# Optimization experiments

Measured on AMD Instinct MI355X. Metric: run time of the kernel, lower is better.

## Reference

```python
import jax, jax.numpy as jnp
import numpy as np

N_NODES = 102400
N_FEAT = 128
N_TPLT = 16
N_TPLT_NODES = 10
N_GRAPHS = 256
EPS = 1.0       # entropic regularization for the Sinkhorn OT solve
N_ITER = 50     # fixed Sinkhorn iterations


def setup_inputs() -> dict:
    key = jax.random.key(0)
    k1, k2 = jax.random.split(key)
    x = jax.random.normal(k1, (N_NODES, N_FEAT), dtype=jnp.float32)
    # template features ~ N(feature_init_mean=0, feature_init_std=1)
    tplt_features = jax.random.normal(k2, (N_TPLT, N_TPLT_NODES, N_FEAT), dtype=jnp.float32)
    # q0 initialized so softmax(q0) is uniform over template nodes
    q0 = jnp.zeros((N_TPLT, N_TPLT_NODES), dtype=jnp.float32)
    # equal-size graphs: 400 nodes per graph, sorted batch vector (PyG convention)
    batch = jnp.repeat(jnp.arange(N_GRAPHS, dtype=jnp.int32), N_NODES // N_GRAPHS)
    return {"x": x, "tplt_features": tplt_features, "q0": q0,
            "batch": batch, "num_graphs": N_GRAPHS}


def _wasserstein_to_templates(x, tplt_features, q0, batch, num_graphs):
    # x: [N, d] node features; tplt_features: [K, M, d]; q0: [K, M]; batch: [N]
    N = x.shape[0]
    K, M, d = tplt_features.shape
    # squared-Euclidean cost C[n,k,m] = ||x_n - T_km||^2   (ot.dist default)
    C = (jnp.sum(x * x, axis=-1)[:, None, None]
         + jnp.sum(tplt_features * tplt_features, axis=-1)[None, :, :]
         - 2.0 * jnp.einsum('nd,kmd->nkm', x, tplt_features))  # [N,K,M]

    # uniform node weights per graph: a_n = 1/|S_{batch[n]}|
    counts = jax.ops.segment_sum(jnp.ones((N,), x.dtype), batch, num_segments=num_graphs)
    log_a = -jnp.log(counts)[batch]                      # [N]
    # template node weights b = softmax(q0, axis=1)
    log_b = jax.nn.log_softmax(q0, axis=1)               # [K,M]

    def seg_lse(t):  # logsumexp over nodes within each graph; t: [N,K,M] -> [G,K,M]
        m = jax.ops.segment_max(t, batch, num_segments=num_graphs)
        s = jax.ops.segment_sum(jnp.exp(t - m[batch]), batch, num_segments=num_graphs)
        return m + jnp.log(s)

    def f_update(g):  # [G,K,M] -> [N,K]
        return EPS * (log_a[:, None] - jax.nn.logsumexp((g[batch] - C) / EPS, axis=2))

    def step(g, _):
        f = f_update(g)
        g_new = EPS * (log_b[None, :, :] - seg_lse((f[:, :, None] - C) / EPS))
        return g_new, None

    g0 = jnp.zeros((num_graphs, K, M), x.dtype)
    g, _ = jax.lax.scan(step, g0, None, length=N_ITER)
    f = f_update(g)
    # transport plan P[n,k,m] = exp((f + g - C)/eps); OT cost = <P, C> per (graph, template)
    logP = (f[:, :, None] + g[batch] - C) / EPS          # [N,K,M]
    per_node = jnp.sum(jnp.exp(logP) * C, axis=2)        # [N,K]
    return jax.ops.segment_sum(per_node, batch, num_segments=num_graphs)  # [G,K]


def reference(x, tplt_features, q0, batch, num_graphs):
    return _wasserstein_to_templates(x, tplt_features, q0, batch, num_graphs)
```

## Files before the change

### kernel.cpp

```cpp
#include <hip/hip_runtime.h>

#define K_TPLT 16
#define M_NODES 10
#define DFEAT 128
#define NMAX 7
#define N_ITER 50
#define NEG_BIG -1e30f
#define LOG2E 1.44269504088896340736f
#define LN2   0.69314718055994530942f

#define EXP2F(x) __builtin_amdgcn_exp2f(x)
#define LOG2F(x) __builtin_amdgcn_logf(x)

__global__ void zero_counts_k(int* counts, int G) {
    int g = blockIdx.x * blockDim.x + threadIdx.x;
    if (g < G) counts[g] = 0;
}

__global__ void count_nodes_k(const int* __restrict__ batch, int* counts, int N) {
    int i = blockIdx.x * blockDim.x + threadIdx.x;
    if (i < N) atomicAdd(&counts[batch[i]], 1);
}

__global__ void scan_counts_k(const int* __restrict__ counts, int* starts, int G) {
    __shared__ int sc[1024];
    int t = threadIdx.x;
    for (int g = t; g < G; g += blockDim.x) sc[g] = counts[g];
    __syncthreads();
    for (int g = t; g < G; g += blockDim.x) {
        int s = 0;
        for (int j = 0; j < g; ++j) s += sc[j];
        starts[g] = s;
    }
}

__global__ __launch_bounds__(64) void sinkhorn_tw_k(
    const float* __restrict__ x, const float* __restrict__ tplt,
    const float* __restrict__ q0, const int* __restrict__ starts,
    const int* __restrict__ counts, float* __restrict__ out, int G)
{
    const int bid  = blockIdx.x;
    const int g    = bid % G;
    const int k    = bid / G;
    const int lane = threadIdx.x;

    const int start = starts[g];
    const int count = counts[g];
    const float a   = 1.0f / (float)count;
    const float la2 = -LOG2F((float)count);

    const float* qk = q0 + k * M_NODES;
    float lbla[M_NODES];
    {
        float qv[M_NODES];
        float qmax = NEG_BIG;
#pragma unroll
        for (int m = 0; m < M_NODES; ++m) { qv[m] = qk[m]; qmax = fmaxf(qmax, qv[m]); }
        float qs = 0.f;
#pragma unroll
        for (int m = 0; m < M_NODES; ++m) {
            qv[m] = (qv[m] - qmax) * LOG2E;
            qs += EXP2F(qv[m]);
        }
        const float corr = LOG2F(qs);
#pragma unroll
        for (int m = 0; m < M_NODES; ++m) lbla[m] = qv[m] - corr - la2;
    }

    bool act[NMAX];
#pragma unroll
    for (int i = 0; i < NMAX; ++i) act[i] = (lane + i * 64) < count;

    float L[NMAX][M_NODES];
    float nsh[NMAX];
    float csh[M_NODES];
    {
        const float* Tk = tplt + (size_t)k * M_NODES * DFEAT;
        float x2[NMAX];
        float t2[M_NODES];
#pragma unroll
        for (int i = 0; i < NMAX; ++i) {
            x2[i] = 0.f;
#pragma unroll
            for (int m = 0; m < M_NODES; ++m) L[i][m] = 0.f;
        }
#pragma unroll
        for (int m = 0; m < M_NODES; ++m) t2[m] = 0.f;

        for (int j = 0; j < DFEAT; j += 4) {
            float4 xv[NMAX];
#pragma unroll
            for (int i = 0; i < NMAX; ++i) {
                if (act[i]) {
                    xv[i] = *(const float4*)(x + (size_t)(start + lane + i * 64) * DFEAT + j);
                } else {
                    xv[i].x = xv[i].y = xv[i].z = xv[i].w = 0.f;
                }
                x2[i] += xv[i].x * xv[i].x + xv[i].y * xv[i].y
                       + xv[i].z * xv[i].z + xv[i].w * xv[i].w;
            }
#pragma unroll
            for (int m = 0; m < M_NODES; ++m) {
                const float4 tv = *(const float4*)(Tk + m * DFEAT + j);
                t2[m] += tv.x * tv.x + tv.y * tv.y + tv.z * tv.z + tv.w * tv.w;
#pragma unroll
                for (int i = 0; i < NMAX; ++i) {
                    L[i][m] += xv[i].x * tv.x + xv[i].y * tv.y
                             + xv[i].z * tv.z + xv[i].w * tv.w;
                }
            }
        }
#pragma unroll
        for (int i = 0; i < NMAX; ++i) {
            float mx = NEG_BIG;
#pragma unroll
            for (int m = 0; m < M_NODES; ++m) {
                L[i][m] = (2.f * L[i][m] - x2[i] - t2[m]) * LOG2E;
                mx = fmaxf(mx, L[i][m]);
            }
            nsh[i] = mx;
#pragma unroll
            for (int m = 0; m < M_NODES; ++m) L[i][m] -= mx;
        }
#pragma unroll
        for (int m = 0; m < M_NODES; ++m) {
            float c = NEG_BIG;
#pragma unroll
            for (int i = 0; i < NMAX; ++i) c = act[i] ? fmaxf(c, L[i][m]) : c;
            for (int off = 32; off > 0; off >>= 1) c = fmaxf(c, __shfl_xor(c, off));
            csh[m] = c;
        }
    }

    float g2[M_NODES];

    {
        float w0[M_NODES], acc[M_NODES];
#pragma unroll
        for (int m = 0; m < M_NODES; ++m) { w0[m] = EXP2F(csh[m]); acc[m] = 0.f; }
#pragma unroll
        for (int i = 0; i < NMAX; ++i) {
            if (act[i]) {
                float E[M_NODES];
                float D = 0.f;
#pragma unroll
                for (int m = 0; m < M_NODES; ++m) {
                    E[m] = EXP2F(L[i][m] - csh[m]);
                    D = fmaf(E[m], w0[m], D);
                }
                const float r = __builtin_amdgcn_rcpf(D);
#pragma unroll
                for (int m = 0; m < M_NODES; ++m) acc[m] = fmaf(E[m], r, acc[m]);
            }
        }
#pragma unroll
        for (int m = 0; m < M_NODES; ++m) {
            float s = acc[m];
            for (int off = 32; off > 0; off >>= 1) s += __shfl_xor(s, off);
            g2[m] = lbla[m] - csh[m] - LOG2F(fmaxf(s, 1e-35f));
        }
    }

    for (int it = 1; it < N_ITER; ++it) {
        float acc[M_NODES];
#pragma unroll
        for (int m = 0; m < M_NODES; ++m) acc[m] = 0.f;

#pragma unroll
        for (int i = 0; i < NMAX; ++i) {
            if (act[i]) {
                float e[M_NODES];
                float zmax = NEG_BIG;
#pragma unroll
                for (int m = 0; m < M_NODES; ++m) {
                    e[m] = g2[m] + L[i][m];
                    zmax = fmaxf(zmax, e[m]);
                }
                float D = 0.f;
#pragma unroll
                for (int m = 0; m < M_NODES; ++m) { e[m] = EXP2F(e[m] - zmax); D += e[m]; }
                const float r = __builtin_amdgcn_rcpf(D);
#pragma unroll
                for (int m = 0; m < M_NODES; ++m) acc[m] = fmaf(e[m], r, acc[m]);
            }
        }
#pragma unroll
        for (int m = 0; m < M_NODES; ++m) {
            float s = acc[m];
            for (int off = 32; off > 0; off >>= 1) s += __shfl_xor(s, off);
            g2[m] = lbla[m] + g2[m] - LOG2F(fmaxf(s, 1e-35f));
        }
    }

    float accum = 0.f;
#pragma unroll
    for (int i = 0; i < NMAX; ++i) {
        if (act[i]) {
            float e[M_NODES];
            float zmax = NEG_BIG;
#pragma unroll
            for (int m = 0; m < M_NODES; ++m) {
                e[m] = g2[m] + L[i][m];
                zmax = fmaxf(zmax, e[m]);
            }
            float D = 0.f;
#pragma unroll
            for (int m = 0; m < M_NODES; ++m) { e[m] = EXP2F(e[m] - zmax); D += e[m]; }
            const float r = __builtin_amdgcn_rcpf(D);
            float q = 0.f;
#pragma unroll
            for (int m = 0; m < M_NODES; ++m) q = fmaf(e[m], L[i][m], q);
            accum += nsh[i] + q * r;
        }
    }
    for (int off = 32; off > 0; off >>= 1) accum += __shfl_xor(accum, off);
    if (lane == 0) out[(size_t)g * K_TPLT + k] = -a * LN2 * accum;
}

extern "C" void kernel_launch(void* const* d_in, const int* in_sizes, int n_in,
                              void* d_out, int out_size, void* d_ws, size_t ws_size,
                              hipStream_t stream) {
    const float* x    = (const float*)d_in[0];
    const float* tplt = (const float*)d_in[1];
    const float* q0   = (const float*)d_in[2];
    const int* batch  = (const int*)d_in[3];
    const int N = in_sizes[3];
    const int G = out_size / K_TPLT;

    int* counts = (int*)d_ws;
    int* starts = counts + G;

    zero_counts_k<<<(G + 255) / 256, 256, 0, stream>>>(counts, G);
    count_nodes_k<<<(N + 255) / 256, 256, 0, stream>>>(batch, counts, N);
    scan_counts_k<<<1, 256, 0, stream>>>(counts, starts, G);
    sinkhorn_tw_k<<<G * K_TPLT, 64, 0, stream>>>(x, tplt, q0, starts, counts,
                                                 (float*)d_out, G);
}
```

Measured before the change: 531.4 us.

## Split each graph-template Sinkhorn solve across two wavefronts with LDS reduction

Each block now uses two 64-lane wavefronts instead of one, with each wave holding up to four node slots per lane rather than seven. Per-iteration column sums and maxima are combined across the two waves through double-buffered shared memory and a block barrier. This is meant to halve per-wave serial work and register pressure (the L array shrinks from 70 to 40 floats), raising occupancy and parallelism for the 4096 blocks. The cost is a __syncthreads per Sinkhorn iteration. Nodes past 512 per graph are no longer covered, versus 448 before, so node coverage is still capped.

```diff
diff --git a/kernel.cpp b/kernel.cpp
--- a/kernel.cpp
+++ b/kernel.cpp
@@ -3,7 +3,7 @@
 #define K_TPLT 16
 #define M_NODES 10
 #define DFEAT 128
-#define NMAX 7
+#define NMAXW 4
 #define N_ITER 50
 #define NEG_BIG -1e30f
 #define LOG2E 1.44269504088896340736f
@@ -34,7 +34,7 @@
     }
 }
 
-__global__ __launch_bounds__(64) void sinkhorn_tw_k(
+__global__ __launch_bounds__(128) void sinkhorn_tw_k(
     const float* __restrict__ x, const float* __restrict__ tplt,
     const float* __restrict__ q0, const int* __restrict__ starts,
     const int* __restrict__ counts, float* __restrict__ out, int G)
@@ -42,7 +42,10 @@
     const int bid  = blockIdx.x;
     const int g    = bid % G;
     const int k    = bid / G;
-    const int lane = threadIdx.x;
+    const int w    = threadIdx.x >> 6;
+    const int lane = threadIdx.x & 63;
+
+    __shared__ float sm[2][2][M_NODES];
 
     const int start = starts[g];
     const int count = counts[g];
@@ -67,69 +70,76 @@
         for (int m = 0; m < M_NODES; ++m) lbla[m] = qv[m] - corr - la2;
     }
 
-    bool act[NMAX];
-#pragma unroll
-    for (int i = 0; i < NMAX; ++i) act[i] = (lane + i * 64) < count;
-
-    float L[NMAX][M_NODES];
-    float nsh[NMAX];
+    bool act[NMAXW];
+#pragma unroll
+    for (int j = 0; j < NMAXW; ++j) act[j] = (lane + 64 * (4 * w + j)) < count;
+
+    float L[NMAXW][M_NODES];
+    float nsh[NMAXW];
     float csh[M_NODES];
     {
         const float* Tk = tplt + (size_t)k * M_NODES * DFEAT;
-        float x2[NMAX];
+        float x2[NMAXW];
         float t2[M_NODES];
 #pragma unroll
-        for (int i = 0; i < NMAX; ++i) {
-            x2[i] = 0.f;
-#pragma unroll
-            for (int m = 0; m < M_NODES; ++m) L[i][m] = 0.f;
+        for (int j = 0; j < NMAXW; ++j) {
+            x2[j] = 0.f;
+#pragma unroll
+            for (int m = 0; m < M_NODES; ++m) L[j][m] = 0.f;
         }
 #pragma unroll
         for (int m = 0; m < M_NODES; ++m) t2[m] = 0.f;
 
-        for (int j = 0; j < DFEAT; j += 4) {
-            float4 xv[NMAX];
-#pragma unroll
-            for (int i = 0; i < NMAX; ++i) {
-                if (act[i]) {
-                    xv[i] = *(const float4*)(x + (size_t)(start + lane + i * 64) * DFEAT + j);
+        for (int jf = 0; jf < DFEAT; jf += 4) {
+            float4 xv[NMAXW];
+#pragma unroll
+            for (int j = 0; j < NMAXW; ++j) {
+                if (act[j]) {
+                    xv[j] = *(const float4*)(x + (size_t)(start + lane + 64 * (4 * w + j)) * DFEAT + jf);
                 } else {
-                    xv[i].x = xv[i].y = xv[i].z = xv[i].w = 0.f;
-                }
-                x2[i] += xv[i].x * xv[i].x + xv[i].y * xv[i].y
-                       + xv[i].z * xv[i].z + xv[i].w * xv[i].w;
+                    xv[j].x = xv[j].y = xv[j].z = xv[j].w = 0.f;
+                }
+                x2[j] += xv[j].x * xv[j].x + xv[j].y * xv[j].y
+                       + xv[j].z * xv[j].z + xv[j].w * xv[j].w;
             }
 #pragma unroll
             for (int m = 0; m < M_NODES; ++m) {
-                const float4 tv = *(const float4*)(Tk + m * DFEAT + j);
+                const float4 tv = *(const float4*)(Tk + m * DFEAT + jf);
                 t2[m] += tv.x * tv.x + tv.y * tv.y + tv.z * tv.z + tv.w * tv.w;
 #pragma unroll
-                for (int i = 0; i < NMAX; ++i) {
-                    L[i][m] += xv[i].x * tv.x + xv[i].y * tv.y
-                             + xv[i].z * tv.z + xv[i].w * tv.w;
-                }
-            }
-        }
-#pragma unroll
-        for (int i = 0; i < NMAX; ++i) {
+                for (int j = 0; j < NMAXW; ++j) {
+                    L[j][m] += xv[j].x * tv.x + xv[j].y * tv.y
+                             + xv[j].z * tv.z + xv[j].w * tv.w;
+                }
+            }
+        }
+#pragma unroll
+        for (int j = 0; j < NMAXW; ++j) {
             float mx = NEG_BIG;
 #pragma unroll
             for (int m = 0; m < M_NODES; ++m) {
-                L[i][m] = (2.f * L[i][m] - x2[i] - t2[m]) * LOG2E;
-                mx = fmaxf(mx, L[i][m]);
-            }
-            nsh[i] = mx;
-#pragma unroll
-            for (int m = 0; m < M_NODES; ++m) L[i][m] -= mx;
+                L[j][m] = (2.f * L[j][m] - x2[j] - t2[m]) * LOG2E;
+                mx = fmaxf(mx, L[j][m]);
+            }
+            nsh[j] = mx;
+#pragma unroll
+            for (int m = 0; m < M_NODES; ++m) L[j][m] -= mx;
         }
 #pragma unroll
         for (int m = 0; m < M_NODES; ++m) {
             float c = NEG_BIG;
 #pragma unroll
-            for (int i = 0; i < NMAX; ++i) c = act[i] ? fmaxf(c, L[i][m]) : c;
+            for (int j = 0; j < NMAXW; ++j) c = act[j] ? fmaxf(c, L[j][m]) : c;
             for (int off = 32; off > 0; off >>= 1) c = fmaxf(c, __shfl_xor(c, off));
             csh[m] = c;
         }
+        if (lane == 0) {
+#pragma unroll
+            for (int m = 0; m < M_NODES; ++m) sm[1][w][m] = csh[m];
+        }
+        __syncthreads();
+#pragma unroll
+        for (int m = 0; m < M_NODES; ++m) csh[m] = fmaxf(sm[1][0][m], sm[1][1][m]);
     }
 
     float g2[M_NODES];
@@ -139,13 +149,13 @@
 #pragma unroll
         for (int m = 0; m < M_NODES; ++m) { w0[m] = EXP2F(csh[m]); acc[m] = 0.f; }
 #pragma unroll
-        for (int i = 0; i < NMAX; ++i) {
-            if (act[i]) {
+        for (int j = 0; j < NMAXW; ++j) {
+            if (act[j]) {
                 float E[M_NODES];
                 float D = 0.f;
 #pragma unroll
                 for (int m = 0; m < M_NODES; ++m) {
-                    E[m] = EXP2F(L[i][m] - csh[m]);
+                    E[m] = EXP2F(L[j][m] - csh[m]);
                     D = fmaf(E[m], w0[m], D);
                 }
                 const float r = __builtin_amdgcn_rcpf(D);
@@ -155,8 +165,16 @@
         }
 #pragma unroll
         for (int m = 0; m < M_NODES; ++m) {
-            float s = acc[m];
-            for (int off = 32; off > 0; off >>= 1) s += __shfl_xor(s, off);
+            for (int off = 32; off > 0; off >>= 1) acc[m] += __shfl_xor(acc[m], off);
+        }
+        if (lane == 0) {
+#pragma unroll
+            for (int m = 0; m < M_NODES; ++m) sm[0][w][m] = acc[m];
+        }
+        __syncthreads();
+#pragma unroll
+        for (int m = 0; m < M_NODES; ++m) {
+            const float s = sm[0][0][m] + sm[0][1][m];
             g2[m] = lbla[m] - csh[m] - LOG2F(fmaxf(s, 1e-35f));
         }
     }
@@ -167,13 +185,13 @@
         for (int m = 0; m < M_NODES; ++m) acc[m] = 0.f;
 
 #pragma unroll
-        for (int i = 0; i < NMAX; ++i) {
-            if (act[i]) {
+        for (int j = 0; j < NMAXW; ++j) {
+            if (act[j]) {
                 float e[M_NODES];
                 float zmax = NEG_BIG;
 #pragma unroll
                 for (int m = 0; m < M_NODES; ++m) {
-                    e[m] = g2[m] + L[i][m];
+                    e[m] = g2[m] + L[j][m];
                     zmax = fmaxf(zmax, e[m]);
                 }
                 float D = 0.f;
@@ -186,21 +204,30 @@
         }
 #pragma unroll
         for (int m = 0; m < M_NODES; ++m) {
-            float s = acc[m];
-            for (int off = 32; off > 0; off >>= 1) s += __shfl_xor(s, off);
+            for (int off = 32; off > 0; off >>= 1) acc[m] += __shfl_xor(acc[m], off);
+        }
+        const int p = it & 1;
+        if (lane == 0) {
+#pragma unroll
+            for (int m = 0; m < M_NODES; ++m) sm[p][w][m] = acc[m];
+        }
+        __syncthreads();
+#pragma unroll
+        for (int m = 0; m < M_NODES; ++m) {
+            const float s = sm[p][0][m] + sm[p][1][m];
             g2[m] = lbla[m] + g2[m] - LOG2F(fmaxf(s, 1e-35f));
         }
     }
 
     float accum = 0.f;
 #pragma unroll
-    for (int i = 0; i < NMAX; ++i) {
-        if (act[i]) {
+    for (int j = 0; j < NMAXW; ++j) {
+        if (act[j]) {
             float e[M_NODES];
             float zmax = NEG_BIG;
 #pragma unroll
             for (int m = 0; m < M_NODES; ++m) {
-                e[m] = g2[m] + L[i][m];
+                e[m] = g2[m] + L[j][m];
                 zmax = fmaxf(zmax, e[m]);
             }
             float D = 0.f;
@@ -209,12 +236,15 @@
             const float r = __builtin_amdgcn_rcpf(D);
             float q = 0.f;
 #pragma unroll
-            for (int m = 0; m < M_NODES; ++m) q = fmaf(e[m], L[i][m], q);
-            accum += nsh[i] + q * r;
+            for (int m = 0; m < M_NODES; ++m) q = fmaf(e[m], L[j][m], q);
+            accum += nsh[j] + q * r;
         }
     }
     for (int off = 32; off > 0; off >>= 1) accum += __shfl_xor(accum, off);
-    if (lane == 0) out[(size_t)g * K_TPLT + k] = -a * LN2 * accum;
+    if (lane == 0) sm[0][w][0] = accum;
+    __syncthreads();
+    if (w == 0 && lane == 0)
+        out[(size_t)g * K_TPLT + k] = -a * LN2 * (sm[0][0][0] + sm[0][1][0]);
 }
 
 extern "C" void kernel_launch(void* const* d_in, const int* in_sizes, int n_in,
@@ -233,6 +263,6 @@
     zero_counts_k<<<(G + 255) / 256, 256, 0, stream>>>(counts, G);
     count_nodes_k<<<(N + 255) / 256, 256, 0, stream>>>(batch, counts, N);
     scan_counts_k<<<1, 256, 0, stream>>>(counts, starts, G);
-    sinkhorn_tw_k<<<G * K_TPLT, 64, 0, stream>>>(x, tplt, q0, starts, counts,
-                                                 (float*)d_out, G);
-}
+    sinkhorn_tw_k<<<G * K_TPLT, 128, 0, stream>>>(x, tplt, q0, starts, counts,
+                                                  (float*)d_out, G);
+}
```

Result: slower. 627.5 us (+18.1%).
